# Kernel tuning notes

Measured on AMD Instinct MI355X. Metric: run time of the kernel, lower is better.

The kernel has to match this reference:

```python
import jax, jax.numpy as jnp
import numpy as np

N = 100000
E = 1600000
IN, HID, OUT = 768, 128, 64


def gcn_conv(x, W, b, src, dst, num_nodes):
    """PyG GCNConv: linear transform, add self-loops, symmetric norm, scatter-add, bias."""
    xw = x @ W  # [N, C_out] (transform before aggregation, as PyG does)
    loops = jnp.arange(num_nodes, dtype=src.dtype)
    s = jnp.concatenate([src, loops])
    d = jnp.concatenate([dst, loops])
    deg = jax.ops.segment_sum(jnp.ones_like(d, dtype=xw.dtype), d, num_segments=num_nodes)
    dis = jnp.where(deg > 0, jax.lax.rsqrt(deg), 0.0)
    norm = dis[s] * dis[d]  # [E+N]
    msg = xw[s] * norm[:, None]  # gather + scale
    out = jax.ops.segment_sum(msg, d, num_segments=num_nodes)  # scatter-add
    return out + b


def setup_inputs() -> dict:
    key = jax.random.key(0)
    ks = jax.random.split(key, 6)
    x = jax.random.normal(ks[0], (N, IN), dtype=jnp.float32)
    edge_index = jax.random.randint(ks[1], (2, E), 0, N, dtype=jnp.int64)
    # Glorot-ish init for GCN weights, zero bias (PyG defaults)
    W1 = jax.random.normal(ks[2], (IN, HID), dtype=jnp.float32) * (1.0 / np.sqrt(IN))
    b1 = jnp.zeros((HID,), dtype=jnp.float32)
    W2 = jax.random.normal(ks[3], (HID, OUT), dtype=jnp.float32) * (1.0 / np.sqrt(HID))
    b2 = jnp.zeros((OUT,), dtype=jnp.float32)
    return {"x": x, "edge_index": edge_index, "W1": W1, "b1": b1, "W2": W2, "b2": b2}


def reference(x, edge_index, W1, b1, W2, b2):
    src, dst = edge_index[0], edge_index[1]
    h = jax.nn.relu(gcn_conv(x, W1, b1, src, dst, N))
    z = gcn_conv(h, W2, b2, src, dst, N)
    return z
```

## Files before the change

kernel.cpp:

```cpp
#include <hip/hip_runtime.h>
#include <hip/hip_bf16.h>


static constexpr int NN    = 100000;
static constexpr int NE    = 1600000;
static constexpr int C_IN  = 768;
static constexpr int C_HID = 128;
static constexpr int C_OUT = 64;
static constexpr int SCAN_B = 256;
static constexpr int NB_SCAN = (NN + SCAN_B - 1) / SCAN_B;

typedef __attribute__((ext_vector_type(8))) short bf16x8;
typedef __attribute__((ext_vector_type(4))) float f32x4;

__device__ __forceinline__ unsigned short f2bf(float f) {
    unsigned int x = __float_as_uint(f);
    unsigned int r = (x + 0x7fffu + ((x >> 16) & 1u)) >> 16;
    return (unsigned short)r;
}
__device__ __forceinline__ float bf2f(unsigned short u) {
    return __uint_as_float(((unsigned int)u) << 16);
}

__global__ void k_zero_i(int* __restrict__ p, int n) {
    int i = blockIdx.x * blockDim.x + threadIdx.x;
    if (i < n) p[i] = 0;
}

__global__ void k_hist(const int* __restrict__ dst, int* __restrict__ cnt, int e) {
    int stride = gridDim.x * blockDim.x;
    for (int i = blockIdx.x * blockDim.x + threadIdx.x; i < e; i += stride)
        atomicAdd(&cnt[dst[i]], 1);
}

__global__ void k_dis(const int* __restrict__ cnt, float* __restrict__ dis, int n) {
    int i = blockIdx.x * blockDim.x + threadIdx.x;
    if (i < n) dis[i] = rsqrtf((float)cnt[i] + 1.0f);
}

__global__ __launch_bounds__(SCAN_B) void k_scan1(const int* __restrict__ cnt,
                                                  int* __restrict__ rp1,
                                                  int* __restrict__ bsum, int n) {
    __shared__ int sh[SCAN_B];
    int b = blockIdx.x, t = threadIdx.x, i = b * SCAN_B + t;
    sh[t] = (i < n) ? cnt[i] : 0;
    __syncthreads();
    for (int off = 1; off < SCAN_B; off <<= 1) {
        int u = (t >= off) ? sh[t - off] : 0;
        __syncthreads();
        sh[t] += u;
        __syncthreads();
    }
    if (i < n) rp1[i] = sh[t];
    if (t == SCAN_B - 1) bsum[b] = sh[t];
}

__global__ __launch_bounds__(512) void k_scan2(int* __restrict__ bsum, int nb) {
    __shared__ int sh[512];
    int t = threadIdx.x;
    sh[t] = (t < nb) ? bsum[t] : 0;
    __syncthreads();
    for (int off = 1; off < 512; off <<= 1) {
        int u = (t >= off) ? sh[t - off] : 0;
        __syncthreads();
        sh[t] += u;
        __syncthreads();
    }
    if (t < nb) bsum[t] = sh[t];
}

__global__ __launch_bounds__(SCAN_B) void k_scan3(int* __restrict__ rowptr,
                                                  const int* __restrict__ bsum,
                                                  int* __restrict__ cursor, int n) {
    int b = blockIdx.x, t = threadIdx.x, i = b * SCAN_B + t;
    if (b == 0 && t == 0) { rowptr[0] = 0; cursor[0] = 0; }
    if (i < n) {
        int v = rowptr[1 + i] + (b > 0 ? bsum[b - 1] : 0);
        rowptr[1 + i] = v;
        if (i + 1 < n) cursor[i + 1] = v;
    }
}

__global__ void k_scatter(const int* __restrict__ src, const int* __restrict__ dst,
                          int* __restrict__ cursor, int* __restrict__ csr, int e) {
    int stride = gridDim.x * blockDim.x;
    for (int i = blockIdx.x * blockDim.x + threadIdx.x; i < e; i += stride) {
        int p = atomicAdd(&cursor[dst[i]], 1);
        csr[p] = src[i];
    }
}

template<int K, int N>
__global__ void k_splitW(const float* __restrict__ W,
                         unsigned short* __restrict__ th,
                         unsigned short* __restrict__ tl) {
    int idx = blockIdx.x * blockDim.x + threadIdx.x;
    if (idx < K * N) {
        int k = idx / N, n = idx - k * N;
        float a = W[idx];
        unsigned short h = f2bf(a);
        th[n * K + k] = h;
        tl[n * K + k] = f2bf(a - bf2f(h));
    }
}

template<int K, int N_>
__global__ __launch_bounds__(256) void k_gemm_mfma(const float* __restrict__ A,
                                                   const unsigned short* __restrict__ Bh,
                                                   const unsigned short* __restrict__ Bl,
                                                   float* __restrict__ C,
                                                   const float* __restrict__ dis, int M) {
    constexpr int RT = (N_ == 128) ? 4 : 2;
    constexpr int CT = 2;
    constexpr int LDK = 40;

    __shared__ unsigned short sAh[64][LDK], sAl[64][LDK];
    __shared__ unsigned short sBh[N_][LDK], sBl[N_][LDK];

    const int tid  = threadIdx.x;
    const int w    = tid >> 6;
    const int lane = tid & 63;
    const int lr   = lane & 15;
    const int ls   = lane >> 4;
    const int row0 = blockIdx.x * 64;

    const int row_base = (N_ == 128) ? 0 : (w >> 1) * 32;
    const int col_base = (N_ == 128) ? w * 32 : (w & 1) * 32;

    f32x4 acc[RT][CT];
    #pragma unroll
    for (int i = 0; i < RT; ++i)
        #pragma unroll
        for (int j = 0; j < CT; ++j) acc[i][j] = (f32x4){0.f, 0.f, 0.f, 0.f};

    for (int k0 = 0; k0 < K; k0 += 32) {
        #pragma unroll
        for (int l = 0; l < 2; ++l) {
            int f   = tid + l * 256;
            int row = f >> 3;
            int kc  = (f & 7) << 2;
            int gr  = row0 + row;
            float4 v = make_float4(0.f, 0.f, 0.f, 0.f);
            if (gr < M) v = *(const float4*)(A + gr * K + k0 + kc);
            unsigned short h0 = f2bf(v.x), h1 = f2bf(v.y), h2 = f2bf(v.z), h3 = f2bf(v.w);
            *(short4*)&sAh[row][kc] = make_short4(h0, h1, h2, h3);
            *(short4*)&sAl[row][kc] = make_short4(f2bf(v.x - bf2f(h0)), f2bf(v.y - bf2f(h1)),
                                                  f2bf(v.z - bf2f(h2)), f2bf(v.w - bf2f(h3)));
        }
        #pragma unroll
        for (int l = 0; l < (N_ * 4) / 256; ++l) {
            int c   = tid + l * 256;
            int col = c >> 2;
            int kc8 = (c & 3) * 8;
            *(uint4*)&sBh[col][kc8] = *(const uint4*)&Bh[col * K + k0 + kc8];
            *(uint4*)&sBl[col][kc8] = *(const uint4*)&Bl[col * K + k0 + kc8];
        }
        __syncthreads();

        bf16x8 ah[RT], al[RT], bh[CT], bl[CT];
        #pragma unroll
        for (int rt = 0; rt < RT; ++rt) {
            int arow = row_base + rt * 16 + lr;
            ah[rt] = *(const bf16x8*)&sAh[arow][ls * 8];
            al[rt] = *(const bf16x8*)&sAl[arow][ls * 8];
        }
        #pragma unroll
        for (int ct = 0; ct < CT; ++ct) {
            int bcol = col_base + ct * 16 + lr;
            bh[ct] = *(const bf16x8*)&sBh[bcol][ls * 8];
            bl[ct] = *(const bf16x8*)&sBl[bcol][ls * 8];
        }
        #pragma unroll
        for (int rt = 0; rt < RT; ++rt)
            #pragma unroll
            for (int ct = 0; ct < CT; ++ct) {
                acc[rt][ct] = __builtin_amdgcn_mfma_f32_16x16x32_bf16(ah[rt], bh[ct], acc[rt][ct], 0, 0, 0);
                acc[rt][ct] = __builtin_amdgcn_mfma_f32_16x16x32_bf16(ah[rt], bl[ct], acc[rt][ct], 0, 0, 0);
                acc[rt][ct] = __builtin_amdgcn_mfma_f32_16x16x32_bf16(al[rt], bh[ct], acc[rt][ct], 0, 0, 0);
            }
        __syncthreads();
    }

    #pragma unroll
    for (int rt = 0; rt < RT; ++rt) {
        #pragma unroll
        for (int r = 0; r < 4; ++r) {
            int grow = row0 + row_base + rt * 16 + ls * 4 + r;
            if (grow < M) {
                float dn = dis[grow];
                #pragma unroll
                for (int ct = 0; ct < CT; ++ct) {
                    int gcol = col_base + ct * 16 + lr;
                    C[grow * N_ + gcol] = acc[rt][ct][r] * dn;
                }
            }
        }
    }
}

template<int C, bool RELU>
__global__ __launch_bounds__(C) void k_agg(const int* __restrict__ rowptr,
                                           const int* __restrict__ csr,
                                           const float* __restrict__ feat,
                                           const float* __restrict__ dis,
                                           const float* __restrict__ bias,
                                           float* __restrict__ out) {
    const int d = blockIdx.x;
    const int c = threadIdx.x;
    const int beg = rowptr[d], end = rowptr[d + 1];
    float sum = feat[d * C + c];
    int e = beg;
    for (; e + 4 <= end; e += 4) {
        int s0 = csr[e], s1 = csr[e + 1], s2 = csr[e + 2], s3 = csr[e + 3];
        float f0 = feat[s0 * C + c], f1 = feat[s1 * C + c];
        float f2 = feat[s2 * C + c], f3 = feat[s3 * C + c];
        sum += (f0 + f1) + (f2 + f3);
    }
    for (; e < end; ++e) sum += feat[csr[e] * C + c];
    float r = sum * dis[d] + bias[c];
    if (RELU) r = fmaxf(r, 0.f);
    out[d * C + c] = r;
}

extern "C" void kernel_launch(void* const* d_in, const int* in_sizes, int n_in,
                              void* d_out, int out_size, void* d_ws, size_t ws_size,
                              hipStream_t stream) {
    const float* x  = (const float*)d_in[0];
    const int*   ei = (const int*)d_in[1];
    const float* W1 = (const float*)d_in[2];
    const float* b1 = (const float*)d_in[3];
    const float* W2 = (const float*)d_in[4];
    const float* b2 = (const float*)d_in[5];
    float* z = (float*)d_out;

    char* ws = (char*)d_ws;
    float* dis    = (float*)(ws + 0);
    int*   cnt    = (int*)  (ws + 524288);
    int*   rowptr = (int*)  (ws + 1048576);
    int*   bsum   = (int*)  (ws + 1572864);
    int*   csr    = (int*)  (ws + 2097152);
    unsigned short* w1h = (unsigned short*)(ws + 8912896);
    unsigned short* w1l = (unsigned short*)(ws + 9109504);
    unsigned short* w2h = (unsigned short*)(ws + 9306112);
    unsigned short* w2l = (unsigned short*)(ws + 9322496);
    float* xw     = (float*)(ws + 9437184);
    float* h      = (float*)(ws + 60817408);

    const int* src = ei;
    const int* dst = ei + NE;

    k_zero_i<<<(NN + 255) / 256, 256, 0, stream>>>(cnt, NN);
    k_hist<<<4096, 256, 0, stream>>>(dst, cnt, NE);
    k_dis<<<(NN + 255) / 256, 256, 0, stream>>>(cnt, dis, NN);
    k_scan1<<<NB_SCAN, SCAN_B, 0, stream>>>(cnt, rowptr + 1, bsum, NN);
    k_scan2<<<1, 512, 0, stream>>>(bsum, NB_SCAN);
    k_scan3<<<NB_SCAN, SCAN_B, 0, stream>>>(rowptr, bsum, cnt , NN);
    k_scatter<<<4096, 256, 0, stream>>>(src, dst, cnt , csr, NE);

    k_splitW<C_IN, C_HID><<<(C_IN * C_HID + 255) / 256, 256, 0, stream>>>(W1, w1h, w1l);
    k_splitW<C_HID, C_OUT><<<(C_HID * C_OUT + 255) / 256, 256, 0, stream>>>(W2, w2h, w2l);

    k_gemm_mfma<C_IN, C_HID><<<(NN + 63) / 64, 256, 0, stream>>>(x, w1h, w1l, xw, dis, NN);
    k_agg<C_HID, true><<<NN, C_HID, 0, stream>>>(rowptr, csr, xw, dis, b1, h);

    float* hw = xw;
    k_gemm_mfma<C_HID, C_OUT><<<(NN + 63) / 64, 256, 0, stream>>>(h, w2h, w2l, hw, dis, NN);
    k_agg<C_OUT, false><<<NN, C_OUT, 0, stream>>>(rowptr, csr, hw, dis, b2, z);
}
```

Before: 895.5 us.

## Store intermediate features in fp16 and vectorize aggregation to 8 channels per thread

The GEMM outputs (xw, hw) and the hidden activation h are now stored as fp16 instead of fp32, which halves the bytes moved by the gather-heavy aggregation kernels and by the second GEMM's input reads. The aggregation kernel is restructured so each thread handles 8 channels via 16-byte vector loads, and each block covers several nodes. The second GEMM gets an fp16-input path. Rounding intermediates to fp16 adds error compared with the fp32 reference.

```diff
diff --git a/kernel.cpp b/kernel.cpp
--- a/kernel.cpp
+++ b/kernel.cpp
@@ -12,6 +12,7 @@
 
 typedef __attribute__((ext_vector_type(8))) short bf16x8;
 typedef __attribute__((ext_vector_type(4))) float f32x4;
+typedef __attribute__((ext_vector_type(8))) _Float16 f16x8;
 
 __device__ __forceinline__ unsigned short f2bf(float f) {
     unsigned int x = __float_as_uint(f);
@@ -104,11 +105,11 @@
     }
 }
 
-template<int K, int N_>
-__global__ __launch_bounds__(256) void k_gemm_mfma(const float* __restrict__ A,
+template<int K, int N_, bool A16>
+__global__ __launch_bounds__(256) void k_gemm_mfma(const void* __restrict__ Ap,
                                                    const unsigned short* __restrict__ Bh,
                                                    const unsigned short* __restrict__ Bl,
-                                                   float* __restrict__ C,
+                                                   _Float16* __restrict__ C,
                                                    const float* __restrict__ dis, int M) {
     constexpr int RT = (N_ == 128) ? 4 : 2;
     constexpr int CT = 2;
@@ -134,18 +135,42 @@
         for (int j = 0; j < CT; ++j) acc[i][j] = (f32x4){0.f, 0.f, 0.f, 0.f};
 
     for (int k0 = 0; k0 < K; k0 += 32) {
-        #pragma unroll
-        for (int l = 0; l < 2; ++l) {
-            int f   = tid + l * 256;
-            int row = f >> 3;
-            int kc  = (f & 7) << 2;
+        if constexpr (!A16) {
+            const float* A = (const float*)Ap;
+            #pragma unroll
+            for (int l = 0; l < 2; ++l) {
+                int f   = tid + l * 256;
+                int row = f >> 3;
+                int kc  = (f & 7) << 2;
+                int gr  = row0 + row;
+                float4 v = make_float4(0.f, 0.f, 0.f, 0.f);
+                if (gr < M) v = *(const float4*)(A + (size_t)gr * K + k0 + kc);
+                unsigned short h0 = f2bf(v.x), h1 = f2bf(v.y), h2 = f2bf(v.z), h3 = f2bf(v.w);
+                *(short4*)&sAh[row][kc] = make_short4(h0, h1, h2, h3);
+                *(short4*)&sAl[row][kc] = make_short4(f2bf(v.x - bf2f(h0)), f2bf(v.y - bf2f(h1)),
+                                                      f2bf(v.z - bf2f(h2)), f2bf(v.w - bf2f(h3)));
+            }
+        } else {
+            const _Float16* A = (const _Float16*)Ap;
+            int f   = tid;
+            int row = f >> 2;
+            int kc  = (f & 3) * 8;
             int gr  = row0 + row;
-            float4 v = make_float4(0.f, 0.f, 0.f, 0.f);
-            if (gr < M) v = *(const float4*)(A + gr * K + k0 + kc);
-            unsigned short h0 = f2bf(v.x), h1 = f2bf(v.y), h2 = f2bf(v.z), h3 = f2bf(v.w);
-            *(short4*)&sAh[row][kc] = make_short4(h0, h1, h2, h3);
-            *(short4*)&sAl[row][kc] = make_short4(f2bf(v.x - bf2f(h0)), f2bf(v.y - bf2f(h1)),
-                                                  f2bf(v.z - bf2f(h2)), f2bf(v.w - bf2f(h3)));
+            f16x8 v;
+            #pragma unroll
+            for (int j = 0; j < 8; ++j) v[j] = (_Float16)0.f;
+            if (gr < M) v = *(const f16x8*)(A + (size_t)gr * K + k0 + kc);
+            unsigned short hh[8], ll[8];
+            #pragma unroll
+            for (int j = 0; j < 8; ++j) {
+                float xv = (float)v[j];
+                hh[j] = f2bf(xv);
+                ll[j] = f2bf(xv - bf2f(hh[j]));
+            }
+            *(short4*)&sAh[row][kc]     = make_short4(hh[0], hh[1], hh[2], hh[3]);
+            *(short4*)&sAh[row][kc + 4] = make_short4(hh[4], hh[5], hh[6], hh[7]);
+            *(short4*)&sAl[row][kc]     = make_short4(ll[0], ll[1], ll[2], ll[3]);
+            *(short4*)&sAl[row][kc + 4] = make_short4(ll[4], ll[5], ll[6], ll[7]);
         }
         #pragma unroll
         for (int l = 0; l < (N_ * 4) / 256; ++l) {
@@ -191,35 +216,67 @@
                 #pragma unroll
                 for (int ct = 0; ct < CT; ++ct) {
                     int gcol = col_base + ct * 16 + lr;
-                    C[grow * N_ + gcol] = acc[rt][ct][r] * dn;
+                    C[(size_t)grow * N_ + gcol] = (_Float16)(acc[rt][ct][r] * dn);
                 }
             }
         }
     }
 }
 
-template<int C, bool RELU>
-__global__ __launch_bounds__(C) void k_agg(const int* __restrict__ rowptr,
-                                           const int* __restrict__ csr,
-                                           const float* __restrict__ feat,
-                                           const float* __restrict__ dis,
-                                           const float* __restrict__ bias,
-                                           float* __restrict__ out) {
-    const int d = blockIdx.x;
-    const int c = threadIdx.x;
+template<int C, bool RELU, bool OUT16>
+__global__ __launch_bounds__(256) void k_aggh(const int* __restrict__ rowptr,
+                                              const int* __restrict__ csr,
+                                              const _Float16* __restrict__ feat,
+                                              const float* __restrict__ dis,
+                                              const float* __restrict__ bias,
+                                              void* __restrict__ outp, int nn) {
+    constexpr int OPR = C / 8;
+    constexpr int NPB = 256 / OPR;
+    const int d = blockIdx.x * NPB + threadIdx.y;
+    if (d >= nn) return;
+    const int o = threadIdx.x;
+
     const int beg = rowptr[d], end = rowptr[d + 1];
-    float sum = feat[d * C + c];
+    float s[8];
+    {
+        f16x8 v = *(const f16x8*)(feat + (size_t)d * C + o * 8);
+        #pragma unroll
+        for (int j = 0; j < 8; ++j) s[j] = (float)v[j];
+    }
     int e = beg;
     for (; e + 4 <= end; e += 4) {
         int s0 = csr[e], s1 = csr[e + 1], s2 = csr[e + 2], s3 = csr[e + 3];
-        float f0 = feat[s0 * C + c], f1 = feat[s1 * C + c];
-        float f2 = feat[s2 * C + c], f3 = feat[s3 * C + c];
-        sum += (f0 + f1) + (f2 + f3);
-    }
-    for (; e < end; ++e) sum += feat[csr[e] * C + c];
-    float r = sum * dis[d] + bias[c];
-    if (RELU) r = fmaxf(r, 0.f);
-    out[d * C + c] = r;
+        f16x8 f0 = *(const f16x8*)(feat + (size_t)s0 * C + o * 8);
+        f16x8 f1 = *(const f16x8*)(feat + (size_t)s1 * C + o * 8);
+        f16x8 f2 = *(const f16x8*)(feat + (size_t)s2 * C + o * 8);
+        f16x8 f3 = *(const f16x8*)(feat + (size_t)s3 * C + o * 8);
+        #pragma unroll
+        for (int j = 0; j < 8; ++j)
+            s[j] += ((float)f0[j] + (float)f1[j]) + ((float)f2[j] + (float)f3[j]);
+    }
+    for (; e < end; ++e) {
+        f16x8 f = *(const f16x8*)(feat + (size_t)csr[e] * C + o * 8);
+        #pragma unroll
+        for (int j = 0; j < 8; ++j) s[j] += (float)f[j];
+    }
+    const float dn = dis[d];
+    float r[8];
+    #pragma unroll
+    for (int j = 0; j < 8; ++j) {
+        r[j] = s[j] * dn + bias[o * 8 + j];
+        if (RELU) r[j] = fmaxf(r[j], 0.f);
+    }
+    if constexpr (OUT16) {
+        _Float16* out = (_Float16*)outp;
+        f16x8 pv;
+        #pragma unroll
+        for (int j = 0; j < 8; ++j) pv[j] = (_Float16)r[j];
+        *(f16x8*)(out + (size_t)d * C + o * 8) = pv;
+    } else {
+        float* out = (float*)outp;
+        *(float4*)(out + (size_t)d * C + o * 8)     = make_float4(r[0], r[1], r[2], r[3]);
+        *(float4*)(out + (size_t)d * C + o * 8 + 4) = make_float4(r[4], r[5], r[6], r[7]);
+    }
 }
 
 extern "C" void kernel_launch(void* const* d_in, const int* in_sizes, int n_in,
@@ -243,8 +300,8 @@
     unsigned short* w1l = (unsigned short*)(ws + 9109504);
     unsigned short* w2h = (unsigned short*)(ws + 9306112);
     unsigned short* w2l = (unsigned short*)(ws + 9322496);
-    float* xw     = (float*)(ws + 9437184);
-    float* h      = (float*)(ws + 60817408);
+    _Float16* xw16 = (_Float16*)(ws + 9437184);
+    _Float16* h16  = (_Float16*)(ws + 41943040);
 
     const int* src = ei;
     const int* dst = ei + NE;
@@ -260,10 +317,18 @@
     k_splitW<C_IN, C_HID><<<(C_IN * C_HID + 255) / 256, 256, 0, stream>>>(W1, w1h, w1l);
     k_splitW<C_HID, C_OUT><<<(C_HID * C_OUT + 255) / 256, 256, 0, stream>>>(W2, w2h, w2l);
 
-    k_gemm_mfma<C_IN, C_HID><<<(NN + 63) / 64, 256, 0, stream>>>(x, w1h, w1l, xw, dis, NN);
-    k_agg<C_HID, true><<<NN, C_HID, 0, stream>>>(rowptr, csr, xw, dis, b1, h);
-
-    float* hw = xw;
-    k_gemm_mfma<C_HID, C_OUT><<<(NN + 63) / 64, 256, 0, stream>>>(h, w2h, w2l, hw, dis, NN);
-    k_agg<C_OUT, false><<<NN, C_OUT, 0, stream>>>(rowptr, csr, hw, dis, b2, z);
-}
+    k_gemm_mfma<C_IN, C_HID, false><<<(NN + 63) / 64, 256, 0, stream>>>(x, w1h, w1l, xw16, dis, NN);
+    {
+        constexpr int NPB = 256 / (C_HID / 8);
+        dim3 blk(C_HID / 8, NPB);
+        k_aggh<C_HID, true, true><<<(NN + NPB - 1) / NPB, blk, 0, stream>>>(rowptr, csr, xw16, dis, b1, h16, NN);
+    }
+
+    _Float16* hw16 = xw16;
+    k_gemm_mfma<C_HID, C_OUT, true><<<(NN + 63) / 64, 256, 0, stream>>>(h16, w2h, w2l, hw16, dis, NN);
+    {
+        constexpr int NPB = 256 / (C_OUT / 8);
+        dim3 blk(C_OUT / 8, NPB);
+        k_aggh<C_OUT, false, false><<<(NN + NPB - 1) / NPB, blk, 0, stream>>>(rowptr, csr, hw16, dis, b2, z, NN);
+    }
+}
```

After: 805.4 us. 1.11x faster.
